# Kernel optimization log

Measured on AMD Instinct MI355X. Metric: run time of the kernel, lower is better.

The kernel has to match this reference:

```python
import jax, jax.numpy as jnp
import numpy as np
import math

H = 2048; NH = 16; HD = 128; E = 8; K = 2; F = 8192; CAP_F = 1.25
B = 2; S = 2048

def _layernorm(x, scale, bias, eps=1e-5):
    m = jnp.mean(x, axis=-1, keepdims=True)
    v = jnp.var(x, axis=-1, keepdims=True)
    return (x - m) * jax.lax.rsqrt(v + eps) * scale + bias

def _rope(x):
    # x: [B, S, NH, HD]; half-split RoPE, theta=10000
    hd = x.shape[-1]
    pos = jnp.arange(x.shape[1], dtype=jnp.float32)
    freqs = 1.0 / (10000.0 ** (jnp.arange(0, hd // 2, dtype=jnp.float32) / (hd // 2)))
    ang = pos[:, None] * freqs[None, :]              # [S, HD/2]
    cos = jnp.cos(ang)[None, :, None, :]
    sin = jnp.sin(ang)[None, :, None, :]
    x1, x2 = jnp.split(x, 2, axis=-1)
    return jnp.concatenate([x1 * cos - x2 * sin, x1 * sin + x2 * cos], axis=-1)

def setup_inputs() -> dict:
    key = jax.random.key(0)
    ks = jax.random.split(key, 16)
    std = 0.02
    inp = {
        'hidden_states': jax.random.normal(ks[0], (B, S, H), jnp.float32),
        'attention_mask': jnp.ones((B, S), jnp.int32),
        'ln1_scale': jnp.ones((H,), jnp.float32), 'ln1_bias': jnp.zeros((H,), jnp.float32),
        'ln2_scale': jnp.ones((H,), jnp.float32), 'ln2_bias': jnp.zeros((H,), jnp.float32),
        'Wq': jax.random.normal(ks[1], (H, NH * HD), jnp.float32) * std,
        'Wk': jax.random.normal(ks[2], (H, NH * HD), jnp.float32) * std,
        'Wv': jax.random.normal(ks[3], (H, NH * HD), jnp.float32) * std,
        'Wo': jax.random.normal(ks[4], (NH * HD, H), jnp.float32) * std,
        'Wg': jax.random.normal(ks[5], (H, H), jnp.float32) * std,
        'bg': jnp.zeros((H,), jnp.float32),
        'ls_attn': jnp.full((H,), 0.1, jnp.float32),
        'ls_moe': jnp.full((H,), 0.1, jnp.float32),
        'router_w': jax.random.normal(ks[6], (H, E), jnp.float32) * std,
        'W1': jax.random.normal(ks[7], (E, H, F), jnp.float32) * std,
        'b1': jnp.zeros((E, F), jnp.float32),
        'W2': jax.random.normal(ks[8], (E, F, H), jnp.float32) * std,
        'b2': jnp.zeros((E, H), jnp.float32),
    }
    return inp

def _forward(hidden_states, attention_mask, ln1_scale, ln1_bias, ln2_scale, ln2_bias,
             Wq, Wk, Wv, Wo, Wg, bg, ls_attn, ls_moe, router_w, W1, b1, W2, b2):
    b, s, h = hidden_states.shape
    # ---- pre-norm MLA attention + residual ----
    xn = _layernorm(hidden_states, ln1_scale, ln1_bias)
    q = (xn @ Wq).reshape(b, s, NH, HD)
    k = (xn @ Wk).reshape(b, s, NH, HD)
    v = (xn @ Wv).reshape(b, s, NH, HD)
    q = _rope(q); k = _rope(k)
    scores = jnp.einsum('bqhd,bkhd->bhqk', q, k) / math.sqrt(HD)
    causal = jnp.tril(jnp.ones((s, s), bool))
    mask = causal[None, None, :, :] & (attention_mask[:, None, None, :] > 0)
    scores = jnp.where(mask, scores, -1e9)
    attn = jax.nn.softmax(scores, axis=-1)
    ctx = jnp.einsum('bhqk,bkhd->bqhd', attn, v).reshape(b, s, NH * HD)
    attn_out = ctx @ Wo
    attn_out = attn_out * jax.nn.sigmoid(xn @ Wg + bg)   # output gating
    attn_out = attn_out * ls_attn                         # layer scale
    hidden_states = hidden_states + attn_out
    # ---- pre-norm MoE FFN + residual ----
    xn2 = _layernorm(hidden_states, ln2_scale, ln2_bias)
    T = b * s
    x = xn2.reshape(T, h)
    logits = (x @ router_w).astype(jnp.float32)           # [T, E]
    probs = jax.nn.softmax(logits, axis=-1)
    gates, idx = jax.lax.top_k(probs, K)                  # [T, K]
    gates = gates / jnp.sum(gates, axis=-1, keepdims=True)
    cap = int(math.ceil(T * K / E * CAP_F))               # expert capacity
    e_flat = idx.reshape(T * K)
    g_flat = gates.reshape(T * K)
    oh = jax.nn.one_hot(e_flat, E, dtype=jnp.int32)       # [TK, E]
    pos = jnp.sum(jnp.cumsum(oh, axis=0) * oh, axis=-1) - 1
    keep = (pos < cap).astype(x.dtype)
    pos_c = jnp.clip(pos, 0, cap - 1)
    x_rep = jnp.repeat(x, K, axis=0)                      # [TK, H]
    buf = jnp.zeros((E, cap, h), x.dtype).at[e_flat, pos_c].add(x_rep * keep[:, None])
    hmid = jax.nn.gelu(jnp.einsum('ech,ehf->ecf', buf, W1) + b1[:, None, :])
    obuf = jnp.einsum('ecf,efh->ech', hmid, W2) + b2[:, None, :]
    tok = obuf[e_flat, pos_c] * (keep * g_flat)[:, None]  # [TK, H]
    moe_out = tok.reshape(T, K, h).sum(axis=1).reshape(b, s, h)
    moe_out = moe_out * ls_moe
    return hidden_states + moe_out

def reference(hidden_states, attention_mask, ln1_scale, ln1_bias, ln2_scale, ln2_bias,
              Wq, Wk, Wv, Wo, Wg, bg, ls_attn, ls_moe, router_w, W1, b1, W2, b2):
    return _forward(hidden_states, attention_mask, ln1_scale, ln1_bias, ln2_scale, ln2_bias,
                    Wq, Wk, Wv, Wo, Wg, bg, ls_attn, ls_moe, router_w, W1, b1, W2, b2)
```

## Files before the change

### kernel.cpp

```cpp
#include <hip/hip_runtime.h>
#include <hip/hip_fp16.h>

typedef _Float16 f16;
typedef _Float16 half4 __attribute__((ext_vector_type(4)));
typedef _Float16 half8 __attribute__((ext_vector_type(8)));
typedef float floatx4 __attribute__((ext_vector_type(4)));

constexpr int kH  = 2048;
constexpr int kS  = 2048;
constexpr int kB  = 2;
constexpr int kT  = kB * kS;
constexpr int kNH = 16;
constexpr int kHD = 128;
constexpr int kE  = 8;
constexpr int kF  = 8192;
constexpr int kCAP = 1280;
constexpr int kTK = kT * 2;

__device__ __forceinline__ void gload16(const void* g, void* lds_) {
  __builtin_amdgcn_global_load_lds((const __attribute__((address_space(1))) void*)g,
                                   (__attribute__((address_space(3))) void*)lds_,
                                   16, 0, 0);
}

__device__ __forceinline__ void xcd_remap(int& bx, int& by, int& bz) {
  const int gx = gridDim.x, gy = gridDim.y;
  const int nwg = gx * gy * gridDim.z;
  int L = (bz * gy + by) * gx + bx;
  L = (L & 7) * (nwg >> 3) + (L >> 3);
  bz = L / (gx * gy);
  const int r = L - bz * gx * gy;
  by = r / gx;  bx = r - by * gx;
}

__global__ __launch_bounds__(256) void transpose_cvt(
    const float* __restrict__ src, f16* __restrict__ dst,
    int ldS, int ldD, long sZ, long dZ)
{
  __shared__ float tile[64][65];
  src += (long)blockIdx.z * sZ;
  dst += (long)blockIdx.z * dZ;
  const int kb = blockIdx.y * 64, nb = blockIdx.x * 64;
  const int tx = threadIdx.x & 15, ty = threadIdx.x >> 4;
#pragma unroll
  for (int i = 0; i < 4; i++) {
    const int r = ty + i * 16;
    const float4 v = *(const float4*)&src[(long)(kb + r) * ldS + nb + tx * 4];
    tile[r][tx * 4 + 0] = v.x; tile[r][tx * 4 + 1] = v.y;
    tile[r][tx * 4 + 2] = v.z; tile[r][tx * 4 + 3] = v.w;
  }
  __syncthreads();
#pragma unroll
  for (int i = 0; i < 4; i++) {
    const int n = ty + i * 16;
    union { f16 h[4]; unsigned long long u; } pk;
#pragma unroll
    for (int j = 0; j < 4; j++) pk.h[j] = (f16)tile[tx * 4 + j][n];
    *(unsigned long long*)&dst[(long)(nb + n) * ldD + kb + tx * 4] = pk.u;
  }
}

__global__ __launch_bounds__(256) void ln_kernel(
    const float* __restrict__ x, const float* __restrict__ sc,
    const float* __restrict__ bi, f16* __restrict__ o16, float* __restrict__ o32)
{
  const long row = blockIdx.x;
  const float* xr = x + row * kH;
  const int t = threadIdx.x;
  const float4 u = ((const float4*)xr)[t * 2];
  const float4 v = ((const float4*)xr)[t * 2 + 1];
  float s = u.x + u.y + u.z + u.w + v.x + v.y + v.z + v.w;
  float q = u.x*u.x + u.y*u.y + u.z*u.z + u.w*u.w + v.x*v.x + v.y*v.y + v.z*v.z + v.w*v.w;
#pragma unroll
  for (int m = 1; m < 64; m <<= 1) { s += __shfl_xor(s, m); q += __shfl_xor(q, m); }
  __shared__ float red_s[4], red_q[4];
  const int w = t >> 6, l = t & 63;
  if (l == 0) { red_s[w] = s; red_q[w] = q; }
  __syncthreads();
  s = red_s[0] + red_s[1] + red_s[2] + red_s[3];
  q = red_q[0] + red_q[1] + red_q[2] + red_q[3];
  const float mean = s * (1.f / kH);
  const float var = q * (1.f / kH) - mean * mean;
  const float rstd = rsqrtf(var + 1e-5f);
  const int c = t * 8;
  const float vals[8] = {u.x, u.y, u.z, u.w, v.x, v.y, v.z, v.w};
#pragma unroll
  for (int j = 0; j < 8; j++) {
    const float y = (vals[j] - mean) * rstd * sc[c + j] + bi[c + j];
    o16[row * kH + c + j] = (f16)y;
    if (o32 != nullptr) o32[row * kH + c + j] = y;
  }
}

#define STG(SRC, TILE, KC, PAR, MAT) { \
  const f16* s_ = (SRC) + (long)(TILE) * 64 + (KC) * 32; \
  char* d_ = lds + ((PAR) * 65536 + (MAT) * 32768 + (KC) * 16384) + ldsW; \
  gload16(s_, d_); \
  gload16(s_ + 128 * ldGl, d_ + 8192); }

#define MROW(MH, MM, AF) \
  acc[(MH)*4+(MM)][0] = __builtin_amdgcn_mfma_f32_16x16x32_f16(AF, bf0, acc[(MH)*4+(MM)][0], 0, 0, 0); \
  acc[(MH)*4+(MM)][1] = __builtin_amdgcn_mfma_f32_16x16x32_f16(AF, bf1, acc[(MH)*4+(MM)][1], 0, 0, 0); \
  acc[(MH)*4+(MM)][2] = __builtin_amdgcn_mfma_f32_16x16x32_f16(AF, bf2, acc[(MH)*4+(MM)][2], 0, 0, 0); \
  acc[(MH)*4+(MM)][3] = __builtin_amdgcn_mfma_f32_16x16x32_f16(AF, bf3, acc[(MH)*4+(MM)][3], 0, 0, 0);

#define PH(PAR, KC, MH, RB, STAGE_STMT, VM_STMT) { \
  const char* au_ = lds + ((PAR) * 65536 + (KC) * 16384); \
  const char* bu_ = lds + ((PAR) * 65536 + 32768 + (KC) * 16384); \
  af0 = *(const half8*)(au_ + afoff + (MH) * 4096 +    0); \
  af1 = *(const half8*)(au_ + afoff + (MH) * 4096 + 1024); \
  af2 = *(const half8*)(au_ + afoff + (MH) * 4096 + 2048); \
  af3 = *(const half8*)(au_ + afoff + (MH) * 4096 + 3072); \
  if (RB) { \
    bf0 = *(const half8*)(bu_ + bfoff +    0); \
    bf1 = *(const half8*)(bu_ + bfoff + 1024); \
    bf2 = *(const half8*)(bu_ + bfoff + 2048); \
    bf3 = *(const half8*)(bu_ + bfoff + 3072); \
  } \
  STAGE_STMT; \
  VM_STMT; \
  __builtin_amdgcn_sched_barrier(0); \
  __builtin_amdgcn_s_barrier(); \
  asm volatile("s_waitcnt lgkmcnt(0)" ::: "memory"); \
  __builtin_amdgcn_sched_barrier(0); \
  __builtin_amdgcn_s_setprio(1); \
  MROW(MH, 0, af0) MROW(MH, 1, af1) MROW(MH, 2, af2) MROW(MH, 3, af3) \
  __builtin_amdgcn_s_setprio(0); }

#define VM10 asm volatile("s_waitcnt vmcnt(10)" ::: "memory")
#define VM8  asm volatile("s_waitcnt vmcnt(8)" ::: "memory")
#define VM4  asm volatile("s_waitcnt vmcnt(4)" ::: "memory")
#define VM0  asm volatile("s_waitcnt vmcnt(0)" ::: "memory")
#define NOP (void)0

template <int EPI, bool SPLITK, bool XCD, bool SWAPXY>
__global__ __launch_bounds__(512, 2) void gemm8p_kernel(
    const f16* __restrict__ A, const f16* __restrict__ B, void* __restrict__ Cv,
    const float* __restrict__ bias, const int* __restrict__ rowCount,
    int M, int N, int K, long ldA, long ldB, long aZ, long bZ, long cZ,
    long cZ2, long biasZ)
{
  int bx = blockIdx.x, by = blockIdx.y, bz = blockIdx.z;
  if (XCD) xcd_remap(bx, by, bz);
  const int bm = SWAPXY ? bx : by;
  const int bn = SWAPXY ? by : bx;
  const int z = bz;
  const int ze = SPLITK ? (z >> 1) : z;
  if (rowCount != nullptr && (int)(bm * 256) >= rowCount[ze]) return;
  __shared__ __align__(16) char lds[131072];
  const long khoff = SPLITK ? (long)(z & 1) * K : 0;
  A += (long)ze * aZ + khoff;  B += (long)ze * bZ + khoff;
  const int tid = threadIdx.x, w = tid >> 6, l = tid & 63;
  const int g = l >> 4, lr = l & 15;
  const long m0 = (long)bm * 256, n0 = (long)bn * 256;
  const int wm = (w >> 2) * 128, wn = (w & 3) * 64;

  floatx4 acc[8][4];
#pragma unroll
  for (int i = 0; i < 8; i++)
#pragma unroll
    for (int j = 0; j < 4; j++) acc[i][j] = floatx4{0.f, 0.f, 0.f, 0.f};

  const int swzS = ((l & 3) * 8) ^ (((l >> 3) & 3) << 3);
  const f16* aSrc;
  const f16* bSrc;
  long ldGl;
  {
    const int srow = w * 16 + (l >> 2);
    aSrc = A + (m0 + srow) * ldA + swzS;
    bSrc = B + (n0 + srow) * ldB + swzS;
  }
  ldGl = ldA;
  const int ldsW = w * 1024;
  const int rsw = (g * 16) ^ (((lr >> 1) & 3) << 4);
  const int afoff = wm * 64 + lr * 64 + rsw;
  const int bfoff = wn * 64 + lr * 64 + rsw;
  half8 af0, af1, af2, af3;
  half8 bf0 = half8{0}, bf1 = half8{0}, bf2 = half8{0}, bf3 = half8{0};

  STG(aSrc, 0, 0, 0, 0);
  STG(bSrc, 0, 0, 0, 1);
  STG(aSrc, 0, 1, 0, 0);
  STG(bSrc, 0, 1, 0, 1);
  STG(bSrc, 1, 0, 1, 1);
  STG(aSrc, 1, 0, 1, 0);
  STG(bSrc, 1, 1, 1, 1);
  VM10;
  __builtin_amdgcn_sched_barrier(0);
  __builtin_amdgcn_s_barrier();

  const int NI = K >> 7;
  for (int i = 0; i < NI - 1; i++) {
    const int t0 = 2 * i, t1 = 2 * i + 1;
    PH(0, 0, 0, 1, STG(aSrc, (t1),     1, 1, 0), VM10)
    PH(0, 0, 1, 0, STG(bSrc, (t0 + 2), 0, 0, 1), VM10)
    PH(0, 1, 0, 1, STG(aSrc, (t0 + 2), 0, 0, 0), VM10)
    PH(0, 1, 1, 0, STG(bSrc, (t0 + 2), 1, 0, 1), VM10)
    PH(1, 0, 0, 1, STG(aSrc, (t0 + 2), 1, 0, 0), VM10)
    PH(1, 0, 1, 0, STG(bSrc, (t1 + 2), 0, 1, 1), VM10)
    PH(1, 1, 0, 1, STG(aSrc, (t1 + 2), 0, 1, 0), VM10)
    PH(1, 1, 1, 0, STG(bSrc, (t1 + 2), 1, 1, 1), VM10)
  }
  {
    const int t1 = 2 * (NI - 1) + 1;
    PH(0, 0, 0, 1, STG(aSrc, (t1), 1, 1, 0), VM8)
    PH(0, 0, 1, 0, NOP, NOP)
    PH(0, 1, 0, 1, NOP, VM4)
    PH(0, 1, 1, 0, NOP, NOP)
    PH(1, 0, 0, 1, NOP, VM0)
    PH(1, 0, 1, 0, NOP, NOP)
    PH(1, 1, 0, 1, NOP, NOP)
    PH(1, 1, 1, 0, NOP, NOP)
  }

  const long crow = m0 + wm + g * 4;
  const long ccol = n0 + wn + lr;
  float* c32 = (float*)Cv + (long)ze * cZ + (SPLITK ? (long)(z & 1) * cZ2 : 0);
  f16* ch = (f16*)Cv + (long)ze * cZ + (SPLITK ? (long)(z & 1) * cZ2 : 0);
#pragma unroll
  for (int mi = 0; mi < 8; mi++)
#pragma unroll
    for (int ni = 0; ni < 4; ni++)
#pragma unroll
      for (int j = 0; j < 4; j++) {
        const long r = crow + mi * 16 + j;
        const long c = ccol + ni * 16;
        float v = acc[mi][ni][j];
        if (EPI == 0) {
          c32[r * N + c] = v;
        } else if (EPI == 2) {
          v += bias[(long)ze * biasZ + c];
          const float u2 = 1.5957691216057308f * (v + 0.044715f * v * v * v);
          const float sg = 1.f / (1.f + __expf(-u2));
          ((f16*)Cv)[(long)ze * cZ + r * N + c] = (f16)(v * sg);
        } else if (EPI == 3) {
          v += bias[(long)ze * biasZ + c];
          ((f16*)Cv)[(long)ze * cZ + r * N + c] = (f16)v;
        } else {
          ch[r * N + c] = (f16)v;
        }
      }
}
#undef STG
#undef MROW
#undef PH
#undef VM10
#undef VM8
#undef VM4
#undef VM0
#undef NOP

__global__ void rope_table_kernel(float* __restrict__ ct, float* __restrict__ st) {
  const int i = blockIdx.x * 256 + threadIdx.x;
  if (i >= kS * 64) return;
  const int s = i >> 6, f = i & 63;
  const double freq = exp(-0.14391156831212787 * (double)f);
  const double ang = (double)s * freq;
  ct[i] = (float)cos(ang);
  st[i] = (float)sin(ang);
}

__global__ __launch_bounds__(256) void rope_kernel(
    const float* __restrict__ q, const float* __restrict__ k,
    const float* __restrict__ ct, const float* __restrict__ st,
    f16* __restrict__ qr, f16* __restrict__ kr)
{
  const long t = blockIdx.x;
  const int s = (int)(t & (kS - 1)), b = (int)(t >> 11);
  for (int u = threadIdx.x; u < kNH * 64; u += 256) {
    const int h = u >> 6, i = u & 63;
    const float c = ct[s * 64 + i], sn = st[s * 64 + i];
    const long src = t * kH + h * kHD + i;
    const long dst = (((long)(b * kNH + h)) * kS + s) * kHD + i;
    float x1 = q[src], x2 = q[src + 64];
    qr[dst]      = (f16)((x1 * c - x2 * sn) * 0.08838834764831845f);
    qr[dst + 64] = (f16)((x1 * sn + x2 * c) * 0.08838834764831845f);
    x1 = k[src]; x2 = k[src + 64];
    kr[dst]      = (f16)(x1 * c - x2 * sn);
    kr[dst + 64] = (f16)(x1 * sn + x2 * c);
  }
}

__global__ __launch_bounds__(256) void attn_kernel(
    const f16* __restrict__ q_r, const f16* __restrict__ k_r,
    const f16* __restrict__ v_t, f16* __restrict__ ctx)
{
  __shared__ f16 Ks[64 * 128];
  __shared__ f16 Vs[128 * 64];
  __shared__ f16 Ps[4][1024];
  int qt = blockIdx.x, h = blockIdx.y, b = blockIdx.z;
  xcd_remap(qt, h, b);
  const int bh = b * kNH + h;
  const int tid = threadIdx.x, w = tid >> 6, l = tid & 63;
  const int g = l >> 4, lr = l & 15;
  const long q0 = (long)qt * 64;
  const f16* qbase = q_r + ((long)bh * kS + q0 + w * 16 + lr) * kHD;
  half8 qf[4];
#pragma unroll
  for (int kc = 0; kc < 4; kc++) qf[kc] = *(const half8*)(qbase + kc * 32 + g * 8);
  floatx4 acc[8];
#pragma unroll
  for (int i = 0; i < 8; i++) acc[i] = floatx4{0.f, 0.f, 0.f, 0.f};
  float mrun[4], lrun[4];
#pragma unroll
  for (int j = 0; j < 4; j++) { mrun[j] = -1e30f; lrun[j] = 0.f; }
  f16* pw = Ps[w];

  for (int kt = 0; kt <= qt; kt++) {
    const long k0 = (long)kt * 64;
#pragma unroll
    for (int c = 0; c < 4; c++) {
      const int cc = w * 4 + c;
      const int row = cc * 4 + (l >> 4);
      const int wb = (l & 15) * 16;
      const int src = (wb ^ ((row & 7) << 4)) >> 1;
      gload16(k_r + ((long)bh * kS + k0 + row) * kHD + src, Ks + cc * 512);
    }
#pragma unroll
    for (int c = 0; c < 4; c++) {
      const int cc = w * 4 + c;
      const int row = cc * 8 + (l >> 3);
      const int wb = (l & 7) * 16;
      const int src = (wb ^ ((row & 7) << 4)) >> 1;
      gload16(v_t + ((long)bh * kHD + row) * kS + k0 + src, Vs + cc * 512);
    }
    asm volatile("s_waitcnt vmcnt(0)" ::: "memory");
    __syncthreads();

    floatx4 sfr[4];
#pragma unroll
    for (int f = 0; f < 4; f++) {
      floatx4 s4 = floatx4{0.f, 0.f, 0.f, 0.f};
      const int row = f * 16 + lr;
#pragma unroll
      for (int kc = 0; kc < 4; kc++) {
        const half8 kfq = *(const half8*)((const char*)Ks + row * 256 +
                            ((kc * 64 + g * 16) ^ ((row & 7) << 4)));
        s4 = __builtin_amdgcn_mfma_f32_16x16x32_f16(qf[kc], kfq, s4, 0, 0, 0);
      }
      sfr[f] = s4;
    }
    if (kt == qt) {
#pragma unroll
      for (int f = 0; f < 4; f++) {
        const int key = kt * 64 + f * 16 + lr;
#pragma unroll
        for (int j = 0; j < 4; j++) {
          const int qrow = qt * 64 + w * 16 + g * 4 + j;
          if (key > qrow) sfr[f][j] = -1e30f;
        }
      }
    }
    float al[4];
#pragma unroll
    for (int j = 0; j < 4; j++) {
      float pm = fmaxf(fmaxf(sfr[0][j], sfr[1][j]), fmaxf(sfr[2][j], sfr[3][j]));
      pm = fmaxf(pm, __shfl_xor(pm, 1)); pm = fmaxf(pm, __shfl_xor(pm, 2));
      pm = fmaxf(pm, __shfl_xor(pm, 4)); pm = fmaxf(pm, __shfl_xor(pm, 8));
      const float mn = fmaxf(mrun[j], pm);
      al[j] = __expf(mrun[j] - mn);
      mrun[j] = mn;
      float rs = 0.f;
#pragma unroll
      for (int f = 0; f < 4; f++) {
        const float p = __expf(sfr[f][j] - mn);
        sfr[f][j] = p; rs += p;
      }
      rs += __shfl_xor(rs, 1); rs += __shfl_xor(rs, 2);
      rs += __shfl_xor(rs, 4); rs += __shfl_xor(rs, 8);
      lrun[j] = lrun[j] * al[j] + rs;
    }
#pragma unroll
    for (int nf = 0; nf < 8; nf++)
#pragma unroll
      for (int j = 0; j < 4; j++) acc[nf][j] *= al[j];
#pragma unroll
    for (int f = 0; f < 4; f++)
#pragma unroll
      for (int j = 0; j < 4; j++) {
        const int row = g * 4 + j;
        const int byteoff = (row * 128 + (f * 16 + lr) * 2) ^ ((row & 7) << 4);
        *(f16*)((char*)pw + byteoff) = (f16)sfr[f][j];
      }
#pragma unroll
    for (int kc = 0; kc < 2; kc++) {
      const half8 pf = *(const half8*)((const char*)pw + lr * 128 +
                         ((kc * 64 + g * 16) ^ ((lr & 7) << 4)));
#pragma unroll
      for (int nf = 0; nf < 8; nf++) {
        const int vrow = nf * 16 + lr;
        const half8 vfr = *(const half8*)((const char*)Vs + vrow * 128 +
                            ((kc * 64 + g * 16) ^ ((vrow & 7) << 4)));
        acc[nf] = __builtin_amdgcn_mfma_f32_16x16x32_f16(pf, vfr, acc[nf], 0, 0, 0);
      }
    }
    __syncthreads();
  }
  const long orow = (long)b * kS + q0 + w * 16;
#pragma unroll
  for (int j = 0; j < 4; j++) {
    const float inv = 1.0f / lrun[j];
    const int r = g * 4 + j;
#pragma unroll
    for (int nf = 0; nf < 8; nf++)
      ctx[(orow + r) * kH + h * kHD + nf * 16 + lr] = (f16)(acc[nf][j] * inv);
  }
}

__global__ __launch_bounds__(256) void combine1_kernel(
    const float* __restrict__ hid, const f16* __restrict__ a0,
    const f16* __restrict__ a1, const float* __restrict__ glin,
    const float* __restrict__ bg, const float* __restrict__ ls,
    float* __restrict__ out)
{
  const long i = (long)blockIdx.x * 256 + threadIdx.x;
  const float4 hv = ((const float4*)hid)[i];
  const half4 av = ((const half4*)a0)[i];
  const half4 aw = ((const half4*)a1)[i];
  const float4 gv = ((const float4*)glin)[i];
  const int c = (int)(i & 511);
  const float4 lv = ((const float4*)ls)[c];
  const float4 bv = ((const float4*)bg)[c];
  float4 o;
  o.x = hv.x + lv.x * ((float)av[0] + (float)aw[0]) / (1.f + __expf(-(gv.x + bv.x)));
  o.y = hv.y + lv.y * ((float)av[1] + (float)aw[1]) / (1.f + __expf(-(gv.y + bv.y)));
  o.z = hv.z + lv.z * ((float)av[2] + (float)aw[2]) / (1.f + __expf(-(gv.z + bv.z)));
  o.w = hv.w + lv.w * ((float)av[3] + (float)aw[3]) / (1.f + __expf(-(gv.w + bv.w)));
  ((float4*)out)[i] = o;
}

__global__ __launch_bounds__(256) void router_kernel(
    const float* __restrict__ x, const float* __restrict__ rw,
    int* __restrict__ eidx, float* __restrict__ gates)
{
  const int t = blockIdx.x * 4 + (threadIdx.x >> 6);
  const int l = threadIdx.x & 63;
  const float* xr = x + (long)t * kH;
  float a[8] = {0.f, 0.f, 0.f, 0.f, 0.f, 0.f, 0.f, 0.f};
  for (int it = 0; it < kH / 64; it++) {
    const float xv = xr[it * 64 + l];
    const float* r = rw + (long)(it * 64 + l) * kE;
#pragma unroll
    for (int e = 0; e < 8; e++) a[e] += xv * r[e];
  }
#pragma unroll
  for (int e = 0; e < 8; e++)
#pragma unroll
    for (int m = 1; m < 64; m <<= 1) a[e] += __shfl_xor(a[e], m);
  if (l == 0) {
    float mx = a[0];
#pragma unroll
    for (int e = 1; e < 8; e++) mx = fmaxf(mx, a[e]);
    float p[8];
#pragma unroll
    for (int e = 0; e < 8; e++) p[e] = __expf(a[e] - mx);
    int i1 = 0; float v1 = p[0];
#pragma unroll
    for (int e = 1; e < 8; e++) if (p[e] > v1) { v1 = p[e]; i1 = e; }
    int i2 = -1; float v2 = -1.f;
#pragma unroll
    for (int e = 0; e < 8; e++) if (e != i1 && p[e] > v2) { v2 = p[e]; i2 = e; }
    const float inv = 1.f / (v1 + v2);
    eidx[t * 2] = i1; eidx[t * 2 + 1] = i2;
    gates[t * 2] = v1 * inv; gates[t * 2 + 1] = v2 * inv;
  }
}

__global__ void scan_kernel(const int* __restrict__ eidx, int* __restrict__ slot,
                            int* __restrict__ counts)
{
  const int l = threadIdx.x;
  int base[8] = {0, 0, 0, 0, 0, 0, 0, 0};
  const unsigned long long lt = (1ull << l) - 1ull;
  for (int it = 0; it < kTK / 64; it++) {
    const int i = it * 64 + l;
    const int e = eidx[i];
    int mypos = 0;
#pragma unroll
    for (int ex = 0; ex < 8; ex++) {
      const unsigned long long mk = __ballot(e == ex);
      if (e == ex) mypos = base[ex] + __popcll(mk & lt);
      base[ex] += __popcll(mk);
    }
    slot[i] = (mypos < kCAP) ? e * kCAP + mypos : -1;
  }
  if (l == 0) {
#pragma unroll
    for (int ex = 0; ex < 8; ex++) counts[ex] = min(base[ex], kCAP);
  }
}

__global__ __launch_bounds__(256) void scatter_kernel(
    const f16* __restrict__ xh, const int* __restrict__ slot, f16* __restrict__ buf)
{
  const int i = blockIdx.x;
  const int s = slot[i];
  if (s < 0) return;
  const long t = i >> 1;
  ((half8*)(buf + (long)s * kH))[threadIdx.x] =
      ((const half8*)(xh + t * kH))[threadIdx.x];
}

__global__ __launch_bounds__(256) void combine2_kernel(
    const float* __restrict__ hid2, const f16* __restrict__ P0,
    const f16* __restrict__ P1, const int* __restrict__ slot,
    const float* __restrict__ gates, const float* __restrict__ b2,
    const float* __restrict__ ls, float* __restrict__ out)
{
  const int t = blockIdx.x;
  const int c = threadIdx.x * 8;
  float m[8] = {0.f, 0.f, 0.f, 0.f, 0.f, 0.f, 0.f, 0.f};
#pragma unroll
  for (int ks = 0; ks < 2; ks++) {
    const int s = slot[t * 2 + ks];
    if (s < 0) continue;
    const float gte = gates[t * 2 + ks];
    const int e = s / kCAP;
    const long ro = (long)s * kH + c;
    const half8 p0 = *(const half8*)&P0[ro];
    const half8 p1 = *(const half8*)&P1[ro];
    const float4 ba = *(const float4*)&b2[e * kH + c];
    const float4 bb = *(const float4*)&b2[e * kH + c + 4];
    m[0] += gte * ((float)p0[0] + (float)p1[0] + ba.x);
    m[1] += gte * ((float)p0[1] + (float)p1[1] + ba.y);
    m[2] += gte * ((float)p0[2] + (float)p1[2] + ba.z);
    m[3] += gte * ((float)p0[3] + (float)p1[3] + ba.w);
    m[4] += gte * ((float)p0[4] + (float)p1[4] + bb.x);
    m[5] += gte * ((float)p0[5] + (float)p1[5] + bb.y);
    m[6] += gte * ((float)p0[6] + (float)p1[6] + bb.z);
    m[7] += gte * ((float)p0[7] + (float)p1[7] + bb.w);
  }
  const float* hp = hid2 + (long)t * kH + c;
  float* op = out + (long)t * kH + c;
#pragma unroll
  for (int j = 0; j < 8; j++) op[j] = hp[j] + ls[c + j] * m[j];
}

extern "C" void kernel_launch(void* const* d_in, const int* in_sizes, int n_in,
                              void* d_out, int out_size, void* d_ws, size_t ws_size,
                              hipStream_t stream)
{
  (void)in_sizes; (void)n_in;
  const float* hidden   = (const float*)d_in[0];
  const float* ln1s     = (const float*)d_in[2];
  const float* ln1b     = (const float*)d_in[3];
  const float* ln2s     = (const float*)d_in[4];
  const float* ln2b     = (const float*)d_in[5];
  const float* Wq       = (const float*)d_in[6];
  const float* Wk       = (const float*)d_in[7];
  const float* Wv       = (const float*)d_in[8];
  const float* Wo       = (const float*)d_in[9];
  const float* Wg       = (const float*)d_in[10];
  const float* bg       = (const float*)d_in[11];
  const float* ls_attn  = (const float*)d_in[12];
  const float* ls_moe   = (const float*)d_in[13];
  const float* router_w = (const float*)d_in[14];
  const float* W1       = (const float*)d_in[15];
  const float* b1       = (const float*)d_in[16];
  const float* W2       = (const float*)d_in[17];
  const float* b2       = (const float*)d_in[18];

  char* ws = (char*)d_ws;
  size_t off = 0;
  auto take = [&](size_t b) { size_t r = off; off += (b + 255) & ~(size_t)255; return r; };
  const size_t o_wT   = take(5ULL * kH * kH * 2);
  const size_t o_w1t  = take((size_t)kE * kF * kH * 2);
  const size_t o_w2t  = take((size_t)kE * kH * kF * 2);
  const size_t o_xn   = take((size_t)kT * kH * 2);
  const size_t o_qkvg = take(4ULL * kT * kH * 4);
  const size_t o_tab  = take(2ULL * kS * 64 * 4);
  const size_t o_qr   = take(3ULL * kT * kH * 2);
  const size_t o_ctx  = take((size_t)kT * kH * 2);
  const size_t o_h2   = take((size_t)kT * kH * 4);
  const size_t o_sm   = take(1 << 20);
  const size_t o_hmid = take((size_t)kE * kCAP * kF * 2);
  if (off > ws_size) { hipMemsetAsync(d_out, 0xFF, (size_t)out_size * 4, stream); return; }

  f16* wT    = (f16*)(ws + o_wT);
  f16* w1t   = (f16*)(ws + o_w1t);
  f16* w2t   = (f16*)(ws + o_w2t);
  f16* xn    = (f16*)(ws + o_xn);
  float* qf  = (float*)(ws + o_qkvg);
  float* kfp = qf + (size_t)kT * kH;
  float* vfp = kfp + (size_t)kT * kH;
  float* gfp = vfp + (size_t)kT * kH;
  float* tabc = (float*)(ws + o_tab);
  float* tabs = tabc + (size_t)kS * 64;
  f16* qr  = (f16*)(ws + o_qr);
  f16* kr  = qr + (size_t)kT * kH;
  f16* vt  = kr + (size_t)kT * kH;
  f16* ctx = (f16*)(ws + o_ctx);
  float* h2 = (float*)(ws + o_h2);
  int* eidx    = (int*)(ws + o_sm);
  float* gates = (float*)(ws + o_sm + 65536);
  int* slot    = (int*)(ws + o_sm + 131072);
  int* counts  = (int*)(ws + o_sm + 196608);
  f16* hmid = (f16*)(ws + o_hmid);
  float* x2f = vfp;
  f16* x2h  = (f16*)(ws + o_qkvg + 1ULL * kT * kH * 4 + (size_t)kT * kH * 2);
  f16* buf  = qr;
  f16* woPh = (f16*)qf;
  f16* P0h = (f16*)(ws + o_w1t);
  f16* P1h = P0h + (size_t)kE * kCAP * kH;

  const long HH = (long)kH * kH;

  transpose_cvt<<<dim3(32, 32, 1), 256, 0, stream>>>(Wq, wT + 0 * HH, kH, kH, 0, 0);
  transpose_cvt<<<dim3(32, 32, 1), 256, 0, stream>>>(Wk, wT + 1 * HH, kH, kH, 0, 0);
  transpose_cvt<<<dim3(32, 32, 1), 256, 0, stream>>>(Wv, wT + 2 * HH, kH, kH, 0, 0);
  transpose_cvt<<<dim3(32, 32, 1), 256, 0, stream>>>(Wg, wT + 3 * HH, kH, kH, 0, 0);
  transpose_cvt<<<dim3(32, 32, 1), 256, 0, stream>>>(Wo, wT + 4 * HH, kH, kH, 0, 0);
  transpose_cvt<<<dim3(kF / 64, kH / 64, kE), 256, 0, stream>>>(
      W1, w1t, kF, kH, (long)kH * kF, (long)kF * kH);
  transpose_cvt<<<dim3(kH / 64, kF / 64, kE), 256, 0, stream>>>(
      W2, w2t, kH, kF, (long)kF * kH, (long)kH * kF);
  ln_kernel<<<kT, 256, 0, stream>>>(hidden, ln1s, ln1b, xn, nullptr);
  gemm8p_kernel<0, false, true, false><<<dim3(kH / 256, kT / 256, 4), 512, 0, stream>>>(
      xn, wT, qf, nullptr, nullptr, kT, kH, kH, kH, kH,
      0L, HH, (long)kT * kH, 0L, 0L);
  rope_table_kernel<<<(kS * 64 + 255) / 256, 256, 0, stream>>>(tabc, tabs);
  rope_kernel<<<kT, 256, 0, stream>>>(qf, kfp, tabc, tabs, qr, kr);
  for (int b = 0; b < kB; b++)
    transpose_cvt<<<dim3(kHD / 64, kS / 64, kNH), 256, 0, stream>>>(
        vfp + (size_t)b * kS * kH, vt + (size_t)b * kNH * kHD * kS,
        kH, kS, 128L, (long)kHD * kS);
  attn_kernel<<<dim3(kS / 64, kNH, kB), 256, 0, stream>>>(qr, kr, vt, ctx);
  gemm8p_kernel<4, true, true, false><<<dim3(kH / 256, kT / 256, 2), 512, 0, stream>>>(
      ctx, wT + 4 * HH, woPh, nullptr, nullptr, kT, kH, 1024, kH, kH,
      0L, 0L, 0L, (long)kT * kH, 0L);
  combine1_kernel<<<(kT * kH / 4) / 256, 256, 0, stream>>>(
      hidden, woPh, woPh + (size_t)kT * kH, gfp, bg, ls_attn, h2);
  ln_kernel<<<kT, 256, 0, stream>>>(h2, ln2s, ln2b, x2h, x2f);
  router_kernel<<<kT / 4, 256, 0, stream>>>(x2f, router_w, eidx, gates);
  scan_kernel<<<1, 64, 0, stream>>>(eidx, slot, counts);
  scatter_kernel<<<kTK, 256, 0, stream>>>(x2h, slot, buf);
  gemm8p_kernel<2, false, false, true><<<dim3(kCAP / 256, kF / 256, kE), 512, 0, stream>>>(
      buf, w1t, hmid, b1, counts, kCAP, kF, kH, kH, kH,
      (long)kCAP * kH, (long)kF * kH, (long)kCAP * kF, 0L, (long)kF);
  gemm8p_kernel<4, true, false, true><<<dim3(kCAP / 256, kH / 256, 2 * kE), 512, 0, stream>>>(
      hmid, w2t, P0h, nullptr, counts, kCAP, kH, 4096, kF, kF,
      (long)kCAP * kF, (long)kH * kF, (long)kCAP * kH, (long)kE * kCAP * kH, 0L);
  combine2_kernel<<<kT, 256, 0, stream>>>(
      h2, P0h, P1h, slot, gates, b2, ls_moe, (float*)d_out);
}
```

Baseline: 1.668 ms.

## Emit QKVG projections in fp16 and widen transpose stores

The QKV/gate GEMM now writes fp16 outputs (EPI 4) instead of fp32, and rope, the V transpose (now a new fp16-to-fp16 transpose kernel) and combine1 read fp16. This halves the intermediate traffic for the four projection outputs. transpose_cvt now writes 16-byte stores instead of 8-byte ones. The SWAPXY template option is removed, so the MoE GEMMs switch to an N-major grid order, which changes tile scheduling and L2 reuse for expert weights. Storing q/k/v/gate in fp16 loses some precision before RoPE and the gate sigmoid.

After: 1.532 ms. 8.1% less time.

```diff
diff --git a/kernel.cpp b/kernel.cpp
--- a/kernel.cpp
+++ b/kernel.cpp
@@ -50,13 +50,40 @@
     tile[r][tx * 4 + 2] = v.z; tile[r][tx * 4 + 3] = v.w;
   }
   __syncthreads();
-#pragma unroll
-  for (int i = 0; i < 4; i++) {
-    const int n = ty + i * 16;
-    union { f16 h[4]; unsigned long long u; } pk;
-#pragma unroll
-    for (int j = 0; j < 4; j++) pk.h[j] = (f16)tile[tx * 4 + j][n];
-    *(unsigned long long*)&dst[(long)(nb + n) * ldD + kb + tx * 4] = pk.u;
+  const int tx8 = threadIdx.x & 7, ty32 = threadIdx.x >> 3;
+#pragma unroll
+  for (int i = 0; i < 2; i++) {
+    const int n = ty32 + i * 32;
+    union { f16 h[8]; float4 v; } pk;
+#pragma unroll
+    for (int j = 0; j < 8; j++) pk.h[j] = (f16)tile[tx8 * 8 + j][n];
+    *(float4*)&dst[(long)(nb + n) * ldD + kb + tx8 * 8] = pk.v;
+  }
+}
+
+__global__ __launch_bounds__(256) void transpose_f16(
+    const f16* __restrict__ src, f16* __restrict__ dst,
+    int ldS, int ldD, long sZ, long dZ)
+{
+  __shared__ f16 tile[64][80];
+  src += (long)blockIdx.z * sZ;
+  dst += (long)blockIdx.z * dZ;
+  const int kb = blockIdx.y * 64, nb = blockIdx.x * 64;
+  const int tx = threadIdx.x & 7, ty = threadIdx.x >> 3;
+#pragma unroll
+  for (int i = 0; i < 2; i++) {
+    const int r = ty + i * 32;
+    *(half8*)&tile[r][tx * 8] =
+        *(const half8*)&src[(long)(kb + r) * ldS + nb + tx * 8];
+  }
+  __syncthreads();
+#pragma unroll
+  for (int i = 0; i < 2; i++) {
+    const int n = ty + i * 32;
+    union { f16 h[8]; float4 v; } pk;
+#pragma unroll
+    for (int j = 0; j < 8; j++) pk.h[j] = tile[tx * 8 + j][n];
+    *(float4*)&dst[(long)(nb + n) * ldD + kb + tx * 8] = pk.v;
   }
 }
 
@@ -133,7 +160,7 @@
 #define VM0  asm volatile("s_waitcnt vmcnt(0)" ::: "memory")
 #define NOP (void)0
 
-template <int EPI, bool SPLITK, bool XCD, bool SWAPXY>
+template <int EPI, bool SPLITK, bool XCD>
 __global__ __launch_bounds__(512, 2) void gemm8p_kernel(
     const f16* __restrict__ A, const f16* __restrict__ B, void* __restrict__ Cv,
     const float* __restrict__ bias, const int* __restrict__ rowCount,
@@ -142,17 +169,15 @@
 {
   int bx = blockIdx.x, by = blockIdx.y, bz = blockIdx.z;
   if (XCD) xcd_remap(bx, by, bz);
-  const int bm = SWAPXY ? bx : by;
-  const int bn = SWAPXY ? by : bx;
   const int z = bz;
   const int ze = SPLITK ? (z >> 1) : z;
-  if (rowCount != nullptr && (int)(bm * 256) >= rowCount[ze]) return;
+  if (rowCount != nullptr && (int)(by * 256) >= rowCount[ze]) return;
   __shared__ __align__(16) char lds[131072];
   const long khoff = SPLITK ? (long)(z & 1) * K : 0;
   A += (long)ze * aZ + khoff;  B += (long)ze * bZ + khoff;
   const int tid = threadIdx.x, w = tid >> 6, l = tid & 63;
   const int g = l >> 4, lr = l & 15;
-  const long m0 = (long)bm * 256, n0 = (long)bn * 256;
+  const long m0 = (long)by * 256, n0 = (long)bx * 256;
   const int wm = (w >> 2) * 128, wn = (w & 3) * 64;
 
   floatx4 acc[8][4];
@@ -261,7 +286,7 @@
 }
 
 __global__ __launch_bounds__(256) void rope_kernel(
-    const float* __restrict__ q, const float* __restrict__ k,
+    const f16* __restrict__ q, const f16* __restrict__ k,
     const float* __restrict__ ct, const float* __restrict__ st,
     f16* __restrict__ qr, f16* __restrict__ kr)
 {
@@ -272,10 +297,10 @@
     const float c = ct[s * 64 + i], sn = st[s * 64 + i];
     const long src = t * kH + h * kHD + i;
     const long dst = (((long)(b * kNH + h)) * kS + s) * kHD + i;
-    float x1 = q[src], x2 = q[src + 64];
+    float x1 = (float)q[src], x2 = (float)q[src + 64];
     qr[dst]      = (f16)((x1 * c - x2 * sn) * 0.08838834764831845f);
     qr[dst + 64] = (f16)((x1 * sn + x2 * c) * 0.08838834764831845f);
-    x1 = k[src]; x2 = k[src + 64];
+    x1 = (float)k[src]; x2 = (float)k[src + 64];
     kr[dst]      = (f16)(x1 * c - x2 * sn);
     kr[dst + 64] = (f16)(x1 * sn + x2 * c);
   }
@@ -409,7 +434,7 @@
 
 __global__ __launch_bounds__(256) void combine1_kernel(
     const float* __restrict__ hid, const f16* __restrict__ a0,
-    const f16* __restrict__ a1, const float* __restrict__ glin,
+    const f16* __restrict__ a1, const f16* __restrict__ glin,
     const float* __restrict__ bg, const float* __restrict__ ls,
     float* __restrict__ out)
 {
@@ -417,15 +442,15 @@
   const float4 hv = ((const float4*)hid)[i];
   const half4 av = ((const half4*)a0)[i];
   const half4 aw = ((const half4*)a1)[i];
-  const float4 gv = ((const float4*)glin)[i];
+  const half4 gv = ((const half4*)glin)[i];
   const int c = (int)(i & 511);
   const float4 lv = ((const float4*)ls)[c];
   const float4 bv = ((const float4*)bg)[c];
   float4 o;
-  o.x = hv.x + lv.x * ((float)av[0] + (float)aw[0]) / (1.f + __expf(-(gv.x + bv.x)));
-  o.y = hv.y + lv.y * ((float)av[1] + (float)aw[1]) / (1.f + __expf(-(gv.y + bv.y)));
-  o.z = hv.z + lv.z * ((float)av[2] + (float)aw[2]) / (1.f + __expf(-(gv.z + bv.z)));
-  o.w = hv.w + lv.w * ((float)av[3] + (float)aw[3]) / (1.f + __expf(-(gv.w + bv.w)));
+  o.x = hv.x + lv.x * ((float)av[0] + (float)aw[0]) / (1.f + __expf(-((float)gv[0] + bv.x)));
+  o.y = hv.y + lv.y * ((float)av[1] + (float)aw[1]) / (1.f + __expf(-((float)gv[1] + bv.y)));
+  o.z = hv.z + lv.z * ((float)av[2] + (float)aw[2]) / (1.f + __expf(-((float)gv[2] + bv.z)));
+  o.w = hv.w + lv.w * ((float)av[3] + (float)aw[3]) / (1.f + __expf(-((float)gv[3] + bv.w)));
   ((float4*)out)[i] = o;
 }
 
@@ -580,10 +605,6 @@
   f16* w1t   = (f16*)(ws + o_w1t);
   f16* w2t   = (f16*)(ws + o_w2t);
   f16* xn    = (f16*)(ws + o_xn);
-  float* qf  = (float*)(ws + o_qkvg);
-  float* kfp = qf + (size_t)kT * kH;
-  float* vfp = kfp + (size_t)kT * kH;
-  float* gfp = vfp + (size_t)kT * kH;
   float* tabc = (float*)(ws + o_tab);
   float* tabs = tabc + (size_t)kS * 64;
   f16* qr  = (f16*)(ws + o_qr);
@@ -596,10 +617,17 @@
   int* slot    = (int*)(ws + o_sm + 131072);
   int* counts  = (int*)(ws + o_sm + 196608);
   f16* hmid = (f16*)(ws + o_hmid);
-  float* x2f = vfp;
-  f16* x2h  = (f16*)(ws + o_qkvg + 1ULL * kT * kH * 4 + (size_t)kT * kH * 2);
+
+  const size_t S2 = (size_t)kT * kH * 2;
+  char* R = ws + o_qkvg;
+  f16* qh = (f16*)(R + 0 * S2);
+  f16* kh = (f16*)(R + 1 * S2);
+  f16* vh = (f16*)(R + 2 * S2);
+  f16* gh = (f16*)(R + 3 * S2);
+  float* x2f = (float*)(R + 4 * S2);
+  f16* x2h   = (f16*)(R + 6 * S2);
+  f16* woPh  = (f16*)(R + 0 * S2);
   f16* buf  = qr;
-  f16* woPh = (f16*)qf;
   f16* P0h = (f16*)(ws + o_w1t);
   f16* P1h = P0h + (size_t)kE * kCAP * kH;
 
@@ -615,29 +643,29 @@
   transpose_cvt<<<dim3(kH / 64, kF / 64, kE), 256, 0, stream>>>(
       W2, w2t, kH, kF, (long)kF * kH, (long)kH * kF);
   ln_kernel<<<kT, 256, 0, stream>>>(hidden, ln1s, ln1b, xn, nullptr);
-  gemm8p_kernel<0, false, true, false><<<dim3(kH / 256, kT / 256, 4), 512, 0, stream>>>(
-      xn, wT, qf, nullptr, nullptr, kT, kH, kH, kH, kH,
+  gemm8p_kernel<4, false, true><<<dim3(kH / 256, kT / 256, 4), 512, 0, stream>>>(
+      xn, wT, qh, nullptr, nullptr, kT, kH, kH, kH, kH,
       0L, HH, (long)kT * kH, 0L, 0L);
   rope_table_kernel<<<(kS * 64 + 255) / 256, 256, 0, stream>>>(tabc, tabs);
-  rope_kernel<<<kT, 256, 0, stream>>>(qf, kfp, tabc, tabs, qr, kr);
+  rope_kernel<<<kT, 256, 0, stream>>>(qh, kh, tabc, tabs, qr, kr);
   for (int b = 0; b < kB; b++)
-    transpose_cvt<<<dim3(kHD / 64, kS / 64, kNH), 256, 0, stream>>>(
-        vfp + (size_t)b * kS * kH, vt + (size_t)b * kNH * kHD * kS,
+    transpose_f16<<<dim3(kHD / 64, kS / 64, kNH), 256, 0, stream>>>(
+        vh + (size_t)b * kS * kH, vt + (size_t)b * kNH * kHD * kS,
         kH, kS, 128L, (long)kHD * kS);
   attn_kernel<<<dim3(kS / 64, kNH, kB), 256, 0, stream>>>(qr, kr, vt, ctx);
-  gemm8p_kernel<4, true, true, false><<<dim3(kH / 256, kT / 256, 2), 512, 0, stream>>>(
+  gemm8p_kernel<4, true, true><<<dim3(kH / 256, kT / 256, 2), 512, 0, stream>>>(
       ctx, wT + 4 * HH, woPh, nullptr, nullptr, kT, kH, 1024, kH, kH,
       0L, 0L, 0L, (long)kT * kH, 0L);
   combine1_kernel<<<(kT * kH / 4) / 256, 256, 0, stream>>>(
-      hidden, woPh, woPh + (size_t)kT * kH, gfp, bg, ls_attn, h2);
+      hidden, woPh, woPh + (size_t)kT * kH, gh, bg, ls_attn, h2);
   ln_kernel<<<kT, 256, 0, stream>>>(h2, ln2s, ln2b, x2h, x2f);
   router_kernel<<<kT / 4, 256, 0, stream>>>(x2f, router_w, eidx, gates);
   scan_kernel<<<1, 64, 0, stream>>>(eidx, slot, counts);
   scatter_kernel<<<kTK, 256, 0, stream>>>(x2h, slot, buf);
-  gemm8p_kernel<2, false, false, true><<<dim3(kCAP / 256, kF / 256, kE), 512, 0, stream>>>(
+  gemm8p_kernel<2, false, false><<<dim3(kF / 256, kCAP / 256, kE), 512, 0, stream>>>(
       buf, w1t, hmid, b1, counts, kCAP, kF, kH, kH, kH,
       (long)kCAP * kH, (long)kF * kH, (long)kCAP * kF, 0L, (long)kF);
-  gemm8p_kernel<4, true, false, true><<<dim3(kCAP / 256, kH / 256, 2 * kE), 512, 0, stream>>>(
+  gemm8p_kernel<4, true, false><<<dim3(kH / 256, kCAP / 256, 2 * kE), 512, 0, stream>>>(
       hmid, w2t, P0h, nullptr, counts, kCAP, kH, 4096, kF, kF,
       (long)kCAP * kF, (long)kH * kF, (long)kCAP * kH, (long)kE * kCAP * kH, 0L);
   combine2_kernel<<<kT, 256, 0, stream>>>(
```
